# Kernel optimization log

Measured on AMD Instinct MI355X. Metric: run time of the kernel, lower is better.

The kernel has to match this reference:

```python
import jax, jax.numpy as jnp
import numpy as np
import itertools

B, RES, RES_, STRIDE = 256, 14, 7, 2
N, N_ = RES * RES, RES_ * RES_
IN_DIM, OUT_DIM = 384, 512
H, KD, AR = 12, 32, 2
D = AR * KD            # 64, per-head value dim
DH = D * H             # 768
NH_KD = KD * H         # 384
KV_H = DH + NH_KD      # 1152
EPS = 1e-5


def _bias_idxs():
    # Replicates the relative-offset indexing from __init__.
    points = list(itertools.product(range(RES), range(RES)))
    points_ = list(itertools.product(range(RES_), range(RES_)))
    offsets, idxs = {}, []
    for p1 in points_:
        for p2 in points:
            off = (abs(p1[0] * STRIDE - p2[0]), abs(p1[1] * STRIDE - p2[1]))
            if off not in offsets:
                offsets[off] = len(offsets)
            idxs.append(offsets[off])
    return np.array(idxs, dtype=np.int32).reshape(N_, N), len(offsets)


def linear_bn(x, w, gamma, beta, mean, var):
    # Linear (no bias) followed by BatchNorm1d in inference form (fused affine).
    s = gamma / jnp.sqrt(var + EPS)
    return jnp.matmul(x, w.T) * s + (beta - mean * s)


def setup_inputs() -> dict:
    key = jax.random.key(0)
    ks = jax.random.split(key, 12)
    idxs_np, n_off = _bias_idxs()

    def bn_params(k, dim):
        k1, k2, k3, k4 = jax.random.split(k, 4)
        return (jax.random.normal(k1, (dim,)) * 0.1 + 1.0,   # gamma
                jax.random.normal(k2, (dim,)) * 0.1,          # beta
                jax.random.normal(k3, (dim,)) * 0.1,          # running_mean
                jax.random.uniform(k4, (dim,), minval=0.5, maxval=1.5))  # running_var

    kv_g, kv_b, kv_m, kv_v = bn_params(ks[1], KV_H)
    q_g, q_b, q_m, q_v = bn_params(ks[3], NH_KD)
    pr_g, pr_b, pr_m, pr_v = bn_params(ks[5], OUT_DIM)

    return {
        "x": jax.random.normal(ks[0], (B, N, IN_DIM), dtype=jnp.float32),
        "kv_w": jax.random.normal(ks[6], (KV_H, IN_DIM), dtype=jnp.float32) * (IN_DIM ** -0.5),
        "kv_g": kv_g, "kv_b": kv_b, "kv_m": kv_m, "kv_v": kv_v,
        "q_w": jax.random.normal(ks[7], (NH_KD, IN_DIM), dtype=jnp.float32) * (IN_DIM ** -0.5),
        "q_g": q_g, "q_b": q_b, "q_m": q_m, "q_v": q_v,
        "proj_w": jax.random.normal(ks[8], (OUT_DIM, DH), dtype=jnp.float32) * (DH ** -0.5),
        "proj_g": pr_g, "proj_b": pr_b, "proj_m": pr_m, "proj_v": pr_v,
        "attention_biases": jax.random.normal(ks[9], (H, n_off), dtype=jnp.float32) * 0.02,
        "bias_idxs": jnp.asarray(idxs_np),
    }


def reference(x, kv_w, kv_g, kv_b, kv_m, kv_v,
              q_w, q_g, q_b, q_m, q_v,
              proj_w, proj_g, proj_b, proj_m, proj_v,
              attention_biases, bias_idxs):
    Bsz = x.shape[0]
    scale = KD ** -0.5
    # kv projection: [B, N, H, KD+D] -> split into k, v
    kv = linear_bn(x, kv_w, kv_g, kv_b, kv_m, kv_v).reshape(Bsz, N, H, KD + D)
    k, v = kv[..., :KD], kv[..., KD:]
    # strided subsample of queries: [B, 14, 14, C] -> [B, 49, C]
    xs = x.reshape(Bsz, RES, RES, IN_DIM)[:, ::STRIDE, ::STRIDE].reshape(Bsz, N_, IN_DIM)
    q = linear_bn(xs, q_w, q_g, q_b, q_m, q_v).reshape(Bsz, N_, H, KD)
    # attention with gathered relative-position bias: bias [H, N_, N]
    bias = attention_biases[:, bias_idxs]
    attn = jnp.einsum('bqhd,bkhd->bhqk', q, k) * scale + bias
    attn = jax.nn.softmax(attn, axis=-1)
    out = jnp.einsum('bhqk,bkhd->bqhd', attn, v).reshape(Bsz, N_, DH)
    out = jax.nn.hard_swish(out)
    return linear_bn(out, proj_w, proj_g, proj_b, proj_m, proj_v)
```

## Files before the change

### kernel.cpp

```cpp
#include <hip/hip_runtime.h>
#include <hip/hip_bf16.h>
#include <math.h>

typedef unsigned short U16;
typedef unsigned int U32;
typedef __attribute__((ext_vector_type(8))) short bf8;
typedef __attribute__((ext_vector_type(4))) float f4;
typedef __attribute__((ext_vector_type(4))) unsigned short u16x4;

#define AS1 __attribute__((address_space(1)))
#define AS3 __attribute__((address_space(3)))

#define BSZ   256
#define NTOK  196
#define NQ    49
#define INDIM 384
#define OUTD  512
#define NH    12
#define DV    64
#define DHD   768
#define KVH   1152
#define NPADR 224

__device__ inline U16 f2bf(float f){
    __hip_bfloat16 h = __float2bfloat16(f);
    return *(U16*)&h;
}
__device__ inline f4 f4zero(){ f4 z; z[0]=0.f; z[1]=0.f; z[2]=0.f; z[3]=0.f; return z; }
__device__ inline bf8 bf8zero(){ bf8 v;
#pragma unroll
    for (int j=0;j<8;++j) v[j]=0; return v; }

__global__ void k_cast8p(const float* __restrict__ in, U16* __restrict__ out, int n8){
    int i = blockIdx.x*256 + threadIdx.x;
    if (i >= n8) return;
    int rall = i / 48;
    int c8   = i - rall*48;
    int b    = rall / NPADR;
    int r    = rall - b*NPADR;
    U16 o[8];
    if (r < NTOK){
        const float* p = in + ((size_t)(b*NTOK + r))*INDIM + c8*8;
#pragma unroll
        for (int j=0;j<8;++j) o[j] = f2bf(p[j]);
    } else {
#pragma unroll
        for (int j=0;j<8;++j) o[j] = 0;
    }
    *(bf8*)(out + (size_t)i*8) = *(const bf8*)o;
}

__global__ void k_castxs(const float* __restrict__ x, U16* __restrict__ out, int n8){
    int i = blockIdx.x*256 + threadIdx.x;
    if (i >= n8) return;
    int row = i / 48;
    int c8  = i - row*48;
    int b   = row / 49;
    int q   = row - b*49;
    int r_  = q / 7, c_ = q - r_*7;
    const float* p = x + ((size_t)(b*NTOK + 28*r_ + 2*c_))*INDIM + c8*8;
    U16 o[8];
#pragma unroll
    for (int j=0;j<8;++j) o[j] = f2bf(p[j]);
    *(bf8*)(out + (size_t)i*8) = *(const bf8*)o;
}

#define W1C (KVH*INDIM/8)
#define W2C (INDIM*INDIM/8)
#define W3C (OUTD*DHD/8)
__global__ void k_castw(const float* __restrict__ w1, const float* __restrict__ w2,
                        const float* __restrict__ w3, U16* __restrict__ o1,
                        U16* __restrict__ o2, U16* __restrict__ o3){
    int i = blockIdx.x*256 + threadIdx.x;
    const float* p; U16* o;
    if (i < W1C){ p = w1 + (size_t)i*8; o = o1 + (size_t)i*8; }
    else if (i < W1C+W2C){ int k=i-W1C; p = w2 + (size_t)k*8; o = o2 + (size_t)k*8; }
    else if (i < W1C+W2C+W3C){ int k=i-W1C-W2C; p = w3 + (size_t)k*8; o = o3 + (size_t)k*8; }
    else return;
    U16 t[8];
#pragma unroll
    for (int j=0;j<8;++j) t[j] = f2bf(p[j]);
    *(bf8*)o = *(const bf8*)t;
}

#define BIAS_N   (NH*NQ*NTOK)
#define BIAS_BLK ((BIAS_N+255)/256)
#define BN_BLK   ((KVH+INDIM+OUTD)/256)
__global__ void k_misc(const float* __restrict__ ab, const int* __restrict__ idxs, int n_off,
                       const float* __restrict__ g1, const float* __restrict__ b1,
                       const float* __restrict__ m1, const float* __restrict__ v1,
                       const float* __restrict__ g2, const float* __restrict__ b2,
                       const float* __restrict__ m2, const float* __restrict__ v2,
                       const float* __restrict__ g3, const float* __restrict__ b3,
                       const float* __restrict__ m3, const float* __restrict__ v3,
                       float* __restrict__ s1, float* __restrict__ bo1,
                       float* __restrict__ s2, float* __restrict__ bo2,
                       float* __restrict__ s3, float* __restrict__ bo3,
                       float* __restrict__ bias_out){
    int blk = blockIdx.x;
    int tid = threadIdx.x;
    if (blk < BIAS_BLK){
        int i = blk*256 + tid;
        if (i < BIAS_N){
            int h = i / (NQ*NTOK);
            int qk = i - h*(NQ*NTOK);
            bias_out[i] = ab[h*n_off + idxs[qk]];
        }
    } else {
        int i = (blk-BIAS_BLK)*256 + tid;
        const float *g,*b,*m,*v; float *so,*bo; int k;
        if (i < KVH){ g=g1;b=b1;m=m1;v=v1;so=s1;bo=bo1;k=i; }
        else if (i < KVH+INDIM){ g=g2;b=b2;m=m2;v=v2;so=s2;bo=bo2;k=i-KVH; }
        else { g=g3;b=b3;m=m3;v=v3;so=s3;bo=bo3;k=i-KVH-INDIM; }
        float s = g[k] / sqrtf(v[k] + 1e-5f);
        so[k] = s;
        bo[k] = b[k] - m[k]*s;
    }
}

__global__ __launch_bounds__(512,2) void k_fused(
    const U16* __restrict__ xbf, const U16* __restrict__ kvw, const U16* __restrict__ qo_,
    const float* __restrict__ skv, const float* __restrict__ bkv,
    const float* __restrict__ biasf, U16* __restrict__ aout)
{
    __shared__ U16 smem[57344];
    const int hw = blockIdx.x;
    const int pair = (hw & 7)*192 + (hw >> 3);
    const int b = pair / 6, hp = pair - b*6;
    const int tid = threadIdx.x, lane = tid & 63, w = tid >> 6;
    const int wm = w & 1, wc = w >> 1;
    const int l15 = lane & 15, oct = lane >> 4;

    U16* Ab[2] = { smem + 0,     smem + 14336 };
    U16* Bb[2] = { smem + 28672, smem + 40960 };

    U32 aoff[4];
#pragma unroll
    for (int c=0;c<3;++c){
        int s = c*512 + tid;
        int ach = s / NPADR, ar = s - ach*NPADR;
        aoff[c] = (U32)(b*NPADR + ar)*INDIM + ach*8;
    }
    if (tid >= 256){
        int s = 1280 + tid;
        int ach = s / NPADR, ar = s - ach*NPADR;
        aoff[3] = (U32)(b*NPADR + ar)*INDIM + ach*8;
    }
    U32 boff[3];
#pragma unroll
    for (int c=0;c<3;++c){
        int s = c*512 + tid;
        int bch = s / 192, br = s - bch*192;
        boff[c] = (U32)(hp*192 + br)*INDIM + bch*8;
    }

    f4 acc[7][3];
#pragma unroll
    for (int i=0;i<7;++i)
#pragma unroll
        for (int j=0;j<3;++j) acc[i][j] = f4zero();

#define STAGE(buf, kb) do{ \
    _Pragma("unroll") \
    for (int c=0;c<3;++c) \
        __builtin_amdgcn_global_load_lds((const AS1 U32*)(xbf + aoff[c] + (kb)), \
            (AS3 U32*)(Ab[buf] + (c*512+tid)*8), 16, 0, 0); \
    if (tid >= 256) \
        __builtin_amdgcn_global_load_lds((const AS1 U32*)(xbf + aoff[3] + (kb)), \
            (AS3 U32*)(Ab[buf] + (1280+tid)*8), 16, 0, 0); \
    _Pragma("unroll") \
    for (int c=0;c<3;++c) \
        __builtin_amdgcn_global_load_lds((const AS1 U32*)(kvw + boff[c] + (kb)), \
            (AS3 U32*)(Bb[buf] + (c*512+tid)*8), 16, 0, 0); \
}while(0)

    STAGE(0, 0);

#pragma unroll
    for (int kt=0; kt<6; ++kt){
        const int cur = kt & 1;
        if (kt < 5){
            STAGE(cur^1, (kt+1)*64);
            if (w < 4) asm volatile("s_waitcnt vmcnt(6)" ::: "memory");
            else       asm volatile("s_waitcnt vmcnt(7)" ::: "memory");
        } else {
            asm volatile("s_waitcnt vmcnt(0)" ::: "memory");
        }
        __builtin_amdgcn_sched_barrier(0);
        __builtin_amdgcn_s_barrier();
        __builtin_amdgcn_sched_barrier(0);

#pragma unroll
        for (int kk=0;kk<2;++kk){
            bf8 af[7], bfr[3];
#pragma unroll
            for (int i=0;i<7;++i)
                af[i]  = *(const bf8*)(Ab[cur] + ((kk*4+oct)*NPADR + wm*112 + i*16 + l15)*8);
#pragma unroll
            for (int j=0;j<3;++j)
                bfr[j] = *(const bf8*)(Bb[cur] + ((kk*4+oct)*192 + wc*48 + j*16 + l15)*8);
            __builtin_amdgcn_s_setprio(1);
#pragma unroll
            for (int i=0;i<7;++i)
#pragma unroll
                for (int j=0;j<3;++j)
                    acc[i][j] = __builtin_amdgcn_mfma_f32_16x16x32_bf16(af[i], bfr[j], acc[i][j], 0, 0, 0);
            __builtin_amdgcn_s_setprio(0);
        }
        __builtin_amdgcn_sched_barrier(0);
        __builtin_amdgcn_s_barrier();
        __builtin_amdgcn_sched_barrier(0);
    }
#undef STAGE

    const int hT = wc >> 1;
    const int hG = hp*2 + hT;
    U16* KLt = smem + hT*28672;
    U16* VLt = KLt + 7168;
#pragma unroll
    for (int j=0;j<3;++j){
        const int cc = (wc&1)*48 + j*16 + l15;
        const float sc = skv[hG*96 + cc];
        const float bi = bkv[hG*96 + cc];
#pragma unroll
        for (int i=0;i<7;++i){
            const int n0 = wm*112 + i*16 + oct*4;
            if (cc < 32){
#pragma unroll
                for (int r=0;r<4;++r)
                    KLt[((cc>>3)*NPADR + n0 + r)*8 + (cc&7)] = f2bf(acc[i][j][r]*sc + bi);
            } else {
                const int dv = cc - 32;
                u16x4 pk;
#pragma unroll
                for (int r=0;r<4;++r) pk[r] = f2bf(acc[i][j][r]*sc + bi);
                *(u16x4*)(VLt + ((n0>>3)*64 + dv)*8 + (oct&1)*4) = pk;
            }
        }
    }
    __syncthreads();

    const int t = w >> 2;
    const int h = hp*2 + t;
    U16* KLa = smem + t*28672;
    U16* VLa = KLa + 7168;
    const int qg = (w&3)*16 + l15;
    bf8 qf = bf8zero();
    if (qg < NQ) qf = *(const bf8*)(qo_ + ((size_t)(b*NQ + qg))*INDIM + h*32 + oct*8);

    f4 sacc[14];
#pragma unroll
    for (int mt=0;mt<14;++mt) sacc[mt] = f4zero();
#pragma unroll
    for (int mt=0;mt<14;++mt){
        const bf8 kf = *(const bf8*)(KLa + (oct*NPADR + mt*16 + l15)*8);
        sacc[mt] = __builtin_amdgcn_mfma_f32_16x16x32_bf16(kf, qf, sacc[mt], 0, 0, 0);
    }

    const float scale = 0.17677669529663689f;
    float mx = -1e30f;
#pragma unroll
    for (int mt=0;mt<14;++mt){
        const int n0 = mt*16 + oct*4;
        f4 bi4 = f4zero();
        if (qg < NQ && n0 < NTOK) bi4 = *(const f4*)(biasf + ((size_t)h*NQ + qg)*NTOK + n0);
#pragma unroll
        for (int r=0;r<4;++r){
            float s = (n0 + r < NTOK) ? sacc[mt][r]*scale + bi4[r] : -1e30f;
            sacc[mt][r] = s;
            mx = fmaxf(mx, s);
        }
    }
    mx = fmaxf(mx, __shfl_xor(mx, 16));
    mx = fmaxf(mx, __shfl_xor(mx, 32));

    float sum = 0.f;
#pragma unroll
    for (int mt=0;mt<14;++mt){
#pragma unroll
        for (int r=0;r<4;++r){
            float p = (mt*16 + oct*4 + r < NTOK) ? __expf(sacc[mt][r] - mx) : 0.f;
            sacc[mt][r] = p;
            sum += p;
        }
    }
    sum += __shfl_xor(sum, 16);
    sum += __shfl_xor(sum, 32);
    const float inv = 1.f / sum;

    __syncthreads();

    const int prow = (w&3)*16 + l15;
    const int pbase = t*28672 + ((prow < 32) ? (21504 + prow*NPADR) : ((prow-32)*NPADR));
    const int psw = prow & 3;
#pragma unroll
    for (int mt=0;mt<14;++mt){
        u16x4 pk;
#pragma unroll
        for (int r=0;r<4;++r) pk[r] = f2bf(sacc[mt][r]*inv);
        const int blk = (mt*2 + (oct>>1)) ^ psw;
        *(u16x4*)(smem + pbase + blk*8 + (oct&1)*4) = pk;
    }

    f4 pacc[4];
#pragma unroll
    for (int dt=0;dt<4;++dt) pacc[dt] = f4zero();
#pragma unroll
    for (int kt=0;kt<7;++kt){
        const bf8 pa = *(const bf8*)(smem + pbase + ((kt*4 + oct) ^ psw)*8);
#pragma unroll
        for (int dt=0;dt<4;++dt){
            const bf8 vf = *(const bf8*)(VLa + ((kt*4 + oct)*64 + dt*16 + l15)*8);
            pacc[dt] = __builtin_amdgcn_mfma_f32_16x16x32_bf16(pa, vf, pacc[dt], 0, 0, 0);
        }
    }

#pragma unroll
    for (int dt=0;dt<4;++dt){
#pragma unroll
        for (int r=0;r<4;++r){
            const int qo2 = (w&3)*16 + oct*4 + r;
            if (qo2 < NQ){
                const int d = dt*16 + l15;
                float v = pacc[dt][r];
                float tt = fminf(fmaxf(v + 3.f, 0.f), 6.f);
                aout[((size_t)(b*NQ + qo2))*DHD + h*DV + d] = f2bf(v * tt * (1.f/6.f));
            }
        }
    }
}

__global__ __launch_bounds__(256,2) void k_qgemm(
    const U16* __restrict__ A, const U16* __restrict__ Bw,
    const float* __restrict__ s_arr, const float* __restrict__ b_arr,
    U16* __restrict__ o16)
{
    __shared__ U16 smem[32768];
    U16* Ab[2] = { smem,          smem + 8192 };
    U16* Bb[2] = { smem + 16384,  smem + 24576 };
    const int gn0 = blockIdx.x * 128;
    const int gm0 = blockIdx.y * 128;
    const int tid  = threadIdx.x;
    const int lane = tid & 63;
    const int w    = tid >> 6;
    const int wm   = w >> 1, wn = w & 1;
    const int l15  = lane & 15, oct = lane >> 4;

    f4 acc[4][4];
#pragma unroll
    for (int i=0;i<4;++i)
#pragma unroll
        for (int j=0;j<4;++j) acc[i][j] = f4zero();

    size_t aoff[4], boff[4];
#pragma unroll
    for (int c=0;c<4;++c){
        int slot = c*256 + tid;
        int row = slot & 127, ch = slot >> 7;
        aoff[c] = (size_t)(gm0 + row)*INDIM + ch*8;
        boff[c] = (size_t)(gn0 + row)*INDIM + ch*8;
    }

#pragma unroll
    for (int c=0;c<4;++c){
        __builtin_amdgcn_global_load_lds((const AS1 U32*)(A + aoff[c]),
            (AS3 U32*)(Ab[0] + (c*256+tid)*8), 16, 0, 0);
        __builtin_amdgcn_global_load_lds((const AS1 U32*)(Bw + boff[c]),
            (AS3 U32*)(Bb[0] + (c*256+tid)*8), 16, 0, 0);
    }

#pragma unroll
    for (int kt=0; kt<6; ++kt){
        const int cur = kt & 1;
        if (kt+1 < 6){
            const int kb = (kt+1)*64;
#pragma unroll
            for (int c=0;c<4;++c){
                __builtin_amdgcn_global_load_lds((const AS1 U32*)(A + aoff[c] + kb),
                    (AS3 U32*)(Ab[cur^1] + (c*256+tid)*8), 16, 0, 0);
                __builtin_amdgcn_global_load_lds((const AS1 U32*)(Bw + boff[c] + kb),
                    (AS3 U32*)(Bb[cur^1] + (c*256+tid)*8), 16, 0, 0);
            }
            asm volatile("s_waitcnt vmcnt(8)" ::: "memory");
        } else {
            asm volatile("s_waitcnt vmcnt(0)" ::: "memory");
        }
        __builtin_amdgcn_sched_barrier(0);
        __builtin_amdgcn_s_barrier();
        __builtin_amdgcn_sched_barrier(0);

#pragma unroll
        for (int kk=0;kk<2;++kk){
            bf8 af[4], bfr[4];
#pragma unroll
            for (int i=0;i<4;++i)
                af[i]  = *(const bf8*)(Ab[cur] + ((kk*4+oct)*128 + wm*64 + i*16 + l15)*8);
#pragma unroll
            for (int j=0;j<4;++j)
                bfr[j] = *(const bf8*)(Bb[cur] + ((kk*4+oct)*128 + wn*64 + j*16 + l15)*8);
            __builtin_amdgcn_s_setprio(1);
#pragma unroll
            for (int i=0;i<4;++i)
#pragma unroll
                for (int j=0;j<4;++j)
                    acc[i][j] = __builtin_amdgcn_mfma_f32_16x16x32_bf16(af[i], bfr[j], acc[i][j], 0, 0, 0);
            __builtin_amdgcn_s_setprio(0);
        }
        __builtin_amdgcn_sched_barrier(0);
        __builtin_amdgcn_s_barrier();
        __builtin_amdgcn_sched_barrier(0);
    }

#pragma unroll
    for (int j=0;j<4;++j){
        const int col = gn0 + wn*64 + j*16 + l15;
        const float sc = s_arr[col];
        const float bi = b_arr[col];
#pragma unroll
        for (int i=0;i<4;++i){
            const int row0 = gm0 + wm*64 + i*16 + oct*4;
#pragma unroll
            for (int r=0;r<4;++r)
                o16[(size_t)(row0+r)*INDIM + col] = f2bf(acc[i][j][r]*sc + bi);
        }
    }
}

__global__ __launch_bounds__(256,2) void k_proj(
    const U16* __restrict__ A, const U16* __restrict__ Bw,
    const float* __restrict__ s_arr, const float* __restrict__ b_arr,
    float* __restrict__ o32)
{
    __shared__ U16 smem[32768];
    U16* Ab[2] = { smem,          smem + 8192 };
    U16* Bb[2] = { smem + 16384,  smem + 24576 };
    const int l   = (blockIdx.x & 7)*49 + (blockIdx.x >> 3);
    const int gn0 = (l & 3) * 128;
    const int gm0 = (l >> 2) * 128;
    const int tid  = threadIdx.x;
    const int lane = tid & 63;
    const int w    = tid >> 6;
    const int wm   = w >> 1, wn = w & 1;
    const int l15  = lane & 15, oct = lane >> 4;

    f4 acc[4][4];
#pragma unroll
    for (int i=0;i<4;++i)
#pragma unroll
        for (int j=0;j<4;++j) acc[i][j] = f4zero();

    size_t aoff[4], boff[4];
#pragma unroll
    for (int c=0;c<4;++c){
        int slot = c*256 + tid;
        int row = slot & 127, ch = slot >> 7;
        aoff[c] = (size_t)(gm0 + row)*DHD + ch*8;
        boff[c] = (size_t)(gn0 + row)*DHD + ch*8;
    }

#pragma unroll
    for (int c=0;c<4;++c){
        __builtin_amdgcn_global_load_lds((const AS1 U32*)(A + aoff[c]),
            (AS3 U32*)(Ab[0] + (c*256+tid)*8), 16, 0, 0);
        __builtin_amdgcn_global_load_lds((const AS1 U32*)(Bw + boff[c]),
            (AS3 U32*)(Bb[0] + (c*256+tid)*8), 16, 0, 0);
    }

#pragma unroll
    for (int kt=0; kt<12; ++kt){
        const int cur = kt & 1;
        if (kt+1 < 12){
            const int kb = (kt+1)*64;
#pragma unroll
            for (int c=0;c<4;++c){
                __builtin_amdgcn_global_load_lds((const AS1 U32*)(A + aoff[c] + kb),
                    (AS3 U32*)(Ab[cur^1] + (c*256+tid)*8), 16, 0, 0);
                __builtin_amdgcn_global_load_lds((const AS1 U32*)(Bw + boff[c] + kb),
                    (AS3 U32*)(Bb[cur^1] + (c*256+tid)*8), 16, 0, 0);
            }
            asm volatile("s_waitcnt vmcnt(8)" ::: "memory");
        } else {
            asm volatile("s_waitcnt vmcnt(0)" ::: "memory");
        }
        __builtin_amdgcn_sched_barrier(0);
        __builtin_amdgcn_s_barrier();
        __builtin_amdgcn_sched_barrier(0);

#pragma unroll
        for (int kk=0;kk<2;++kk){
            bf8 af[4], bfr[4];
#pragma unroll
            for (int i=0;i<4;++i)
                af[i]  = *(const bf8*)(Ab[cur] + ((kk*4+oct)*128 + wm*64 + i*16 + l15)*8);
#pragma unroll
            for (int j=0;j<4;++j)
                bfr[j] = *(const bf8*)(Bb[cur] + ((kk*4+oct)*128 + wn*64 + j*16 + l15)*8);
            __builtin_amdgcn_s_setprio(1);
#pragma unroll
            for (int i=0;i<4;++i)
#pragma unroll
                for (int j=0;j<4;++j)
                    acc[i][j] = __builtin_amdgcn_mfma_f32_16x16x32_bf16(af[i], bfr[j], acc[i][j], 0, 0, 0);
            __builtin_amdgcn_s_setprio(0);
        }
        __builtin_amdgcn_sched_barrier(0);
        __builtin_amdgcn_s_barrier();
        __builtin_amdgcn_sched_barrier(0);
    }

#pragma unroll
    for (int j=0;j<4;++j){
        const int col = gn0 + wn*64 + j*16 + l15;
        const float sc = s_arr[col];
        const float bi = b_arr[col];
#pragma unroll
        for (int i=0;i<4;++i){
            const int row0 = gm0 + wm*64 + i*16 + oct*4;
#pragma unroll
            for (int r=0;r<4;++r)
                o32[(size_t)(row0+r)*OUTD + col] = acc[i][j][r]*sc + bi;
        }
    }
}

extern "C" void kernel_launch(void* const* d_in, const int* in_sizes, int n_in,
                              void* d_out, int out_size, void* d_ws, size_t ws_size,
                              hipStream_t stream)
{
    const float* x    = (const float*)d_in[0];
    const float* kv_w = (const float*)d_in[1];
    const float* kv_g = (const float*)d_in[2];
    const float* kv_b = (const float*)d_in[3];
    const float* kv_m = (const float*)d_in[4];
    const float* kv_v = (const float*)d_in[5];
    const float* q_w  = (const float*)d_in[6];
    const float* q_g  = (const float*)d_in[7];
    const float* q_b  = (const float*)d_in[8];
    const float* q_m  = (const float*)d_in[9];
    const float* q_v  = (const float*)d_in[10];
    const float* pr_w = (const float*)d_in[11];
    const float* pr_g = (const float*)d_in[12];
    const float* pr_b = (const float*)d_in[13];
    const float* pr_m = (const float*)d_in[14];
    const float* pr_v = (const float*)d_in[15];
    const float* ab   = (const float*)d_in[16];
    const int*  idxs  = (const int*)d_in[17];
    const int n_off = in_sizes[16] / NH;

    char* ws = (char*)d_ws;
    size_t off = 0;
    auto alloc = [&](size_t bytes)->char*{
        char* p = ws + off; off += (bytes + 255) & ~(size_t)255; return p;
    };
    U16*   x_bf   = (U16*)  alloc((size_t)BSZ*NPADR*INDIM*2);
    U16*   xs_bf  = (U16*)  alloc((size_t)BSZ*NQ*INDIM*2);
    U16*   kvw_bf = (U16*)  alloc((size_t)KVH*INDIM*2);
    U16*   qw_bf  = (U16*)  alloc((size_t)INDIM*INDIM*2);
    U16*   prw_bf = (U16*)  alloc((size_t)OUTD*DHD*2);
    float* s_kv   = (float*)alloc(KVH*4);
    float* b_kv   = (float*)alloc(KVH*4);
    float* s_q    = (float*)alloc(INDIM*4);
    float* b_q    = (float*)alloc(INDIM*4);
    float* s_pr   = (float*)alloc(OUTD*4);
    float* b_pr   = (float*)alloc(OUTD*4);
    float* biasf  = (float*)alloc(((size_t)NH*NQ*NTOK + 256)*4);
    U16*   q_out  = (U16*)  alloc((size_t)BSZ*NQ*INDIM*2);
    U16*   a_out  = (U16*)  alloc((size_t)BSZ*NQ*DHD*2);
    if (off > ws_size) return;

    {
        int n8 = BSZ*NPADR*INDIM/8;
        k_cast8p<<<(n8+255)/256, 256, 0, stream>>>(x, x_bf, n8);
    }
    {
        int n8 = BSZ*NQ*INDIM/8;
        k_castxs<<<(n8+255)/256, 256, 0, stream>>>(x, xs_bf, n8);
    }
    k_castw<<<(W1C+W2C+W3C+255)/256, 256, 0, stream>>>(kv_w, q_w, pr_w, kvw_bf, qw_bf, prw_bf);
    k_misc<<<BIAS_BLK+BN_BLK, 256, 0, stream>>>(
        ab, idxs, n_off,
        kv_g, kv_b, kv_m, kv_v, q_g, q_b, q_m, q_v, pr_g, pr_b, pr_m, pr_v,
        s_kv, b_kv, s_q, b_q, s_pr, b_pr, biasf);

    {
        dim3 g(INDIM/128, BSZ*NQ/128);
        k_qgemm<<<g, 256, 0, stream>>>(xs_bf, qw_bf, s_q, b_q, q_out);
    }
    k_fused<<<BSZ*NH/2, 512, 0, stream>>>(x_bf, kvw_bf, q_out, s_kv, b_kv, biasf, a_out);
    k_proj<<<392, 256, 0, stream>>>(a_out, prw_bf, s_pr, b_pr, (float*)d_out);
}
```

Before: 200.4 us.

## Split fused attention kernel to one head per 256-thread block

The fused KV-projection plus attention kernel now handles one (batch, head) per 256-thread block instead of two heads per 512-thread block, and the grid doubles to match. Shared memory per block shrinks, and the P buffer no longer overlaps the K region, which removes one block-wide barrier. The aim is better occupancy and scheduling granularity. In exchange, the x tile for each batch is loaded once per head instead of once per head pair, so global and L2 traffic for the A operand doubles.

```diff
diff --git a/kernel.cpp b/kernel.cpp
--- a/kernel.cpp
+++ b/kernel.cpp
@@ -118,40 +118,40 @@
     }
 }
 
-__global__ __launch_bounds__(512,2) void k_fused(
+#define FA1 14336
+#define FB0 28672
+#define FB1 34816
+#define VL  7168
+#define PL  21504
+__global__ __launch_bounds__(256,2) void k_fused(
     const U16* __restrict__ xbf, const U16* __restrict__ kvw, const U16* __restrict__ qo_,
     const float* __restrict__ skv, const float* __restrict__ bkv,
     const float* __restrict__ biasf, U16* __restrict__ aout)
 {
-    __shared__ U16 smem[57344];
+    __shared__ U16 smem[40960];
     const int hw = blockIdx.x;
-    const int pair = (hw & 7)*192 + (hw >> 3);
-    const int b = pair / 6, hp = pair - b*6;
+    const int bh = (hw & 7)*384 + (hw >> 3);
+    const int b = bh / NH, h = bh - b*NH;
     const int tid = threadIdx.x, lane = tid & 63, w = tid >> 6;
-    const int wm = w & 1, wc = w >> 1;
+    const int wm = w & 1, wn = w >> 1;
     const int l15 = lane & 15, oct = lane >> 4;
 
-    U16* Ab[2] = { smem + 0,     smem + 14336 };
-    U16* Bb[2] = { smem + 28672, smem + 40960 };
-
-    U32 aoff[4];
-#pragma unroll
-    for (int c=0;c<3;++c){
-        int s = c*512 + tid;
+    U16* Ab[2] = { smem + 0,   smem + FA1 };
+    U16* Bb[2] = { smem + FB0, smem + FB1 };
+
+    U32 aoff[7];
+#pragma unroll
+    for (int c=0;c<7;++c){
+        int s = c*256 + tid;
         int ach = s / NPADR, ar = s - ach*NPADR;
         aoff[c] = (U32)(b*NPADR + ar)*INDIM + ach*8;
     }
-    if (tid >= 256){
-        int s = 1280 + tid;
-        int ach = s / NPADR, ar = s - ach*NPADR;
-        aoff[3] = (U32)(b*NPADR + ar)*INDIM + ach*8;
-    }
     U32 boff[3];
 #pragma unroll
     for (int c=0;c<3;++c){
-        int s = c*512 + tid;
-        int bch = s / 192, br = s - bch*192;
-        boff[c] = (U32)(hp*192 + br)*INDIM + bch*8;
+        int s = c*256 + tid;
+        int bch = s / 96, br = s - bch*96;
+        boff[c] = (U32)(h*96 + br)*INDIM + bch*8;
     }
 
     f4 acc[7][3];
@@ -162,16 +162,13 @@
 
 #define STAGE(buf, kb) do{ \
     _Pragma("unroll") \
-    for (int c=0;c<3;++c) \
+    for (int c=0;c<7;++c) \
         __builtin_amdgcn_global_load_lds((const AS1 U32*)(xbf + aoff[c] + (kb)), \
-            (AS3 U32*)(Ab[buf] + (c*512+tid)*8), 16, 0, 0); \
-    if (tid >= 256) \
-        __builtin_amdgcn_global_load_lds((const AS1 U32*)(xbf + aoff[3] + (kb)), \
-            (AS3 U32*)(Ab[buf] + (1280+tid)*8), 16, 0, 0); \
+            (AS3 U32*)(Ab[buf] + (c*256+tid)*8), 16, 0, 0); \
     _Pragma("unroll") \
     for (int c=0;c<3;++c) \
         __builtin_amdgcn_global_load_lds((const AS1 U32*)(kvw + boff[c] + (kb)), \
-            (AS3 U32*)(Bb[buf] + (c*512+tid)*8), 16, 0, 0); \
+            (AS3 U32*)(Bb[buf] + (c*256+tid)*8), 16, 0, 0); \
 }while(0)
 
     STAGE(0, 0);
@@ -181,8 +178,7 @@
         const int cur = kt & 1;
         if (kt < 5){
             STAGE(cur^1, (kt+1)*64);
-            if (w < 4) asm volatile("s_waitcnt vmcnt(6)" ::: "memory");
-            else       asm volatile("s_waitcnt vmcnt(7)" ::: "memory");
+            asm volatile("s_waitcnt vmcnt(10)" ::: "memory");
         } else {
             asm volatile("s_waitcnt vmcnt(0)" ::: "memory");
         }
@@ -198,7 +194,7 @@
                 af[i]  = *(const bf8*)(Ab[cur] + ((kk*4+oct)*NPADR + wm*112 + i*16 + l15)*8);
 #pragma unroll
             for (int j=0;j<3;++j)
-                bfr[j] = *(const bf8*)(Bb[cur] + ((kk*4+oct)*192 + wc*48 + j*16 + l15)*8);
+                bfr[j] = *(const bf8*)(Bb[cur] + ((kk*4+oct)*96 + wn*48 + j*16 + l15)*8);
             __builtin_amdgcn_s_setprio(1);
 #pragma unroll
             for (int i=0;i<7;++i)
@@ -213,38 +209,30 @@
     }
 #undef STAGE
 
-    const int hT = wc >> 1;
-    const int hG = hp*2 + hT;
-    U16* KLt = smem + hT*28672;
-    U16* VLt = KLt + 7168;
 #pragma unroll
     for (int j=0;j<3;++j){
-        const int cc = (wc&1)*48 + j*16 + l15;
-        const float sc = skv[hG*96 + cc];
-        const float bi = bkv[hG*96 + cc];
+        const int cc = wn*48 + j*16 + l15;
+        const float sc = skv[h*96 + cc];
+        const float bi = bkv[h*96 + cc];
 #pragma unroll
         for (int i=0;i<7;++i){
             const int n0 = wm*112 + i*16 + oct*4;
             if (cc < 32){
 #pragma unroll
                 for (int r=0;r<4;++r)
-                    KLt[((cc>>3)*NPADR + n0 + r)*8 + (cc&7)] = f2bf(acc[i][j][r]*sc + bi);
+                    smem[((cc>>3)*NPADR + n0 + r)*8 + (cc&7)] = f2bf(acc[i][j][r]*sc + bi);
             } else {
                 const int dv = cc - 32;
                 u16x4 pk;
 #pragma unroll
                 for (int r=0;r<4;++r) pk[r] = f2bf(acc[i][j][r]*sc + bi);
-                *(u16x4*)(VLt + ((n0>>3)*64 + dv)*8 + (oct&1)*4) = pk;
+                *(u16x4*)(smem + VL + ((n0>>3)*64 + dv)*8 + (oct&1)*4) = pk;
             }
         }
     }
     __syncthreads();
 
-    const int t = w >> 2;
-    const int h = hp*2 + t;
-    U16* KLa = smem + t*28672;
-    U16* VLa = KLa + 7168;
-    const int qg = (w&3)*16 + l15;
+    const int qg = w*16 + l15;
     bf8 qf = bf8zero();
     if (qg < NQ) qf = *(const bf8*)(qo_ + ((size_t)(b*NQ + qg))*INDIM + h*32 + oct*8);
 
@@ -253,7 +241,7 @@
     for (int mt=0;mt<14;++mt) sacc[mt] = f4zero();
 #pragma unroll
     for (int mt=0;mt<14;++mt){
-        const bf8 kf = *(const bf8*)(KLa + (oct*NPADR + mt*16 + l15)*8);
+        const bf8 kf = *(const bf8*)(smem + (oct*NPADR + mt*16 + l15)*8);
         sacc[mt] = __builtin_amdgcn_mfma_f32_16x16x32_bf16(kf, qf, sacc[mt], 0, 0, 0);
     }
 
@@ -288,10 +276,8 @@
     sum += __shfl_xor(sum, 32);
     const float inv = 1.f / sum;
 
-    __syncthreads();
-
-    const int prow = (w&3)*16 + l15;
-    const int pbase = t*28672 + ((prow < 32) ? (21504 + prow*NPADR) : ((prow-32)*NPADR));
+    const int prow = w*16 + l15;
+    const int pbase = PL + prow*NPADR;
     const int psw = prow & 3;
 #pragma unroll
     for (int mt=0;mt<14;++mt){
@@ -310,7 +296,7 @@
         const bf8 pa = *(const bf8*)(smem + pbase + ((kt*4 + oct) ^ psw)*8);
 #pragma unroll
         for (int dt=0;dt<4;++dt){
-            const bf8 vf = *(const bf8*)(VLa + ((kt*4 + oct)*64 + dt*16 + l15)*8);
+            const bf8 vf = *(const bf8*)(smem + VL + ((kt*4 + oct)*64 + dt*16 + l15)*8);
             pacc[dt] = __builtin_amdgcn_mfma_f32_16x16x32_bf16(pa, vf, pacc[dt], 0, 0, 0);
         }
     }
@@ -319,7 +305,7 @@
     for (int dt=0;dt<4;++dt){
 #pragma unroll
         for (int r=0;r<4;++r){
-            const int qo2 = (w&3)*16 + oct*4 + r;
+            const int qo2 = w*16 + oct*4 + r;
             if (qo2 < NQ){
                 const int d = dt*16 + l15;
                 float v = pacc[dt][r];
@@ -586,6 +572,6 @@
         dim3 g(INDIM/128, BSZ*NQ/128);
         k_qgemm<<<g, 256, 0, stream>>>(xs_bf, qw_bf, s_q, b_q, q_out);
     }
-    k_fused<<<BSZ*NH/2, 512, 0, stream>>>(x_bf, kvw_bf, q_out, s_kv, b_kv, biasf, a_out);
+    k_fused<<<BSZ*NH, 256, 0, stream>>>(x_bf, kvw_bf, q_out, s_kv, b_kv, biasf, a_out);
     k_proj<<<392, 256, 0, stream>>>(a_out, prw_bf, s_pr, b_pr, (float*)d_out);
 }
```

Result: no change. 197.1 us (-1.6%).
